# Performance work log

Measured on AMD Instinct MI355X. Metric: run time of the kernel, lower is better.

Reference implementation:

```python
import jax, jax.numpy as jnp
import numpy as np

EMBED_DIM = 1024
NUM_HEADS = 16
HEAD_DIM = EMBED_DIM // NUM_HEADS


def setup_inputs() -> dict:
    key = jax.random.key(0)
    ks = jax.random.split(key, 9)
    B, S, E = 2, 2048, EMBED_DIM
    scale = 1.0 / np.sqrt(E)
    return {
        "query": jax.random.normal(ks[0], (B, S, E), jnp.float32),
        "key": jax.random.normal(ks[1], (B, S, E), jnp.float32),
        "value": jax.random.normal(ks[2], (B, S, E), jnp.float32),
        "wq": jax.random.normal(ks[3], (E, E), jnp.float32) * scale,
        "bq": jnp.zeros((E,), jnp.float32),
        "wk": jax.random.normal(ks[4], (E, E), jnp.float32) * scale,
        "bk": jnp.zeros((E,), jnp.float32),
        "wv": jax.random.normal(ks[5], (E, E), jnp.float32) * scale,
        "bv": jnp.zeros((E,), jnp.float32),
    }


def _split_heads(x):
    B, S, _ = x.shape
    return x.reshape(B, S, NUM_HEADS, HEAD_DIM).transpose(0, 2, 1, 3)  # [B,H,S,Dh]


def reference(query, key, value, wq, bq, wk, bk, wv, bv):
    q = _split_heads(query @ wq + bq)   # [B,H,S,Dh]
    k = _split_heads(key @ wk + bk)
    v = _split_heads(value @ wv + bv)
    logits = jnp.einsum("bhqd,bhkd->bhqk", q, k) / jnp.sqrt(
        jnp.asarray(HEAD_DIM, q.dtype)
    )
    attn = jax.nn.softmax(logits, axis=-1)          # [B,H,S,S]
    out = jnp.einsum("bhqk,bhkd->bhqd", attn, v)    # [B,H,S,Dh]
    B, H, S, Dh = out.shape
    out = out.transpose(0, 2, 1, 3).reshape(B, S, H * Dh)  # [B,S,E]
    return out, attn
```

## Files before the change

kernel.cpp:

```cpp
#include <hip/hip_runtime.h>

typedef float  f32x4  __attribute__((ext_vector_type(4)));
typedef int    i32x4  __attribute__((ext_vector_type(4)));
typedef short  bf16x8 __attribute__((ext_vector_type(8)));
typedef short  s16x4  __attribute__((ext_vector_type(4)));

#define NB   2
#define SEQ  2048
#define EMB  1024
#define NH   16
#define DH   64
#define MATN (NB * SEQ * EMB)

__device__ inline short f2bf(float f) {
    unsigned u = __float_as_uint(f);
    u += 0x7fffu + ((u >> 16) & 1u);
    return (short)(u >> 16);
}

__device__ inline unsigned cvtpk(float lo, float hi) {
    unsigned r;
    asm("v_cvt_pk_bf16_f32 %0, %1, %2" : "=v"(r) : "v"(lo), "v"(hi));
    return r;
}

__device__ inline float fexp2(float x) {
#if __has_builtin(__builtin_amdgcn_exp2f)
    return __builtin_amdgcn_exp2f(x);
#else
    return exp2f(x);
#endif
}

__device__ inline f32x4 mfma16(bf16x8 a, bf16x8 b, f32x4 c) {
    return __builtin_amdgcn_mfma_f32_16x16x32_bf16(a, b, c, 0, 0, 0);
}

__global__ __launch_bounds__(256) void prep_kernel(const float* __restrict__ q,
                                                   const float* __restrict__ k,
                                                   const float* __restrict__ v,
                                                   const float* __restrict__ w0,
                                                   const float* __restrict__ w1,
                                                   const float* __restrict__ w2,
                                                   short* __restrict__ wt,
                                                   short* __restrict__ abf) {
    int blk = blockIdx.x;
    int t = threadIdx.x;
    if (blk < 3072) {
        __shared__ float tile[32][33];
        int mat = blk >> 10;
        int rem = blk & 1023;
        int kt = rem >> 5, nt = rem & 31;
        const float* W = (mat == 0) ? w0 : ((mat == 1) ? w1 : w2);
        int row = t >> 3, c4 = (t & 7) << 2;

        f32x4 val = *(const f32x4*)(W + (kt * 32 + row) * EMB + nt * 32 + c4);
        tile[row][c4 + 0] = val[0];
        tile[row][c4 + 1] = val[1];
        tile[row][c4 + 2] = val[2];
        tile[row][c4 + 3] = val[3];
        __syncthreads();

        int n = nt * 32 + row;
        s16x4 o;
        o[0] = f2bf(tile[c4 + 0][row]);
        o[1] = f2bf(tile[c4 + 1][row]);
        o[2] = f2bf(tile[c4 + 2][row]);
        o[3] = f2bf(tile[c4 + 3][row]);
        *(s16x4*)(wt + mat * (EMB * EMB) + n * EMB + kt * 32 + c4) = o;
    } else {
        long long i = (long long)(blk - 3072) * 2048 + t * 8;
        int mat = (int)(i >> 22);
        int off = (int)(i & (MATN - 1));
        const float* A = (mat == 0) ? q : ((mat == 1) ? k : v);
        f32x4 x = *(const f32x4*)(A + off);
        f32x4 y = *(const f32x4*)(A + off + 4);
        bf16x8 pk;
        pk[0] = f2bf(x[0]); pk[1] = f2bf(x[1]); pk[2] = f2bf(x[2]); pk[3] = f2bf(x[3]);
        pk[4] = f2bf(y[0]); pk[5] = f2bf(y[1]); pk[6] = f2bf(y[2]); pk[7] = f2bf(y[3]);
        *(bf16x8*)(abf + i) = pk;
    }
}

template <bool BF16A>
__global__ __launch_bounds__(256) void proj_kernel(const short* __restrict__ abf,
                                                   const float* __restrict__ a0,
                                                   const float* __restrict__ a1,
                                                   const float* __restrict__ a2,
                                                   const float* __restrict__ b0,
                                                   const float* __restrict__ b1,
                                                   const float* __restrict__ b2,
                                                   const short* __restrict__ wt,
                                                   short* __restrict__ qkv) {
    __shared__ __align__(16) short smem[2][128][72];
    short (*abuf)[72] = smem[0];
    short (*wbuf)[72] = smem[1];

    int orig = blockIdx.x;
    int blk = (orig & 7) * 96 + (orig >> 3);
    int mat = blk >> 8;
    int rem = blk & 255;
    int mt = rem >> 3, nt = rem & 7;

    const float* bias = (mat == 0) ? b0 : ((mat == 1) ? b1 : b2);
    const float* Af = (mat == 0) ? a0 : ((mat == 1) ? a1 : a2);
    const short* Ab = abf + mat * MATN;
    const short* WT = wt + mat * (EMB * EMB);
    short* O = qkv + mat * MATN;
    float scale = (mat == 0) ? 0.125f * 1.44269504f : 1.0f;

    int t = threadIdx.x;
    int lane = t & 63, w = t >> 6;
    int wr = w >> 1, wc = w & 1;
    int lg = lane >> 4, lm = lane & 15;

    int m0 = mt * 128, n0 = nt * 128;
    int srow = t >> 1, koff = (t & 1) * 32;

    f32x4 acc[4][4] = {};

    for (int k0 = 0; k0 < EMB; k0 += 64) {
        if constexpr (BF16A) {
            const short* ap = Ab + (m0 + srow) * EMB + k0 + koff;
#pragma unroll
            for (int i = 0; i < 4; i++)
                *(i32x4*)&abuf[srow][koff + i * 8] = *(const i32x4*)(ap + i * 8);
        } else {
            const float* ap = Af + (m0 + srow) * EMB + k0 + koff;
#pragma unroll
            for (int i = 0; i < 4; i++) {
                f32x4 x = *(const f32x4*)(ap + i * 8);
                f32x4 y = *(const f32x4*)(ap + i * 8 + 4);
                bf16x8 pk;
                pk[0] = f2bf(x[0]); pk[1] = f2bf(x[1]); pk[2] = f2bf(x[2]); pk[3] = f2bf(x[3]);
                pk[4] = f2bf(y[0]); pk[5] = f2bf(y[1]); pk[6] = f2bf(y[2]); pk[7] = f2bf(y[3]);
                *(bf16x8*)&abuf[srow][koff + i * 8] = pk;
            }
        }
        const short* wp = WT + (n0 + srow) * EMB + k0 + koff;
#pragma unroll
        for (int i = 0; i < 4; i++)
            *(i32x4*)&wbuf[srow][koff + i * 8] = *(const i32x4*)(wp + i * 8);
        __syncthreads();
#pragma unroll
        for (int ks = 0; ks < 2; ks++) {
            bf16x8 af[4], bfr[4];
#pragma unroll
            for (int mi = 0; mi < 4; mi++)
                af[mi] = *(const bf16x8*)&abuf[wr * 64 + mi * 16 + lm][ks * 32 + lg * 8];
#pragma unroll
            for (int ni = 0; ni < 4; ni++)
                bfr[ni] = *(const bf16x8*)&wbuf[wc * 64 + ni * 16 + lm][ks * 32 + lg * 8];
#pragma unroll
            for (int mi = 0; mi < 4; mi++)
#pragma unroll
                for (int ni = 0; ni < 4; ni++)
                    acc[mi][ni] = mfma16(af[mi], bfr[ni], acc[mi][ni]);
        }
        __syncthreads();
    }

    int bidx = m0 >> 11;
    if (mat == 2) {
#pragma unroll
        for (int ni = 0; ni < 4; ni++) {
            int e = n0 + wc * 64 + ni * 16 + lm;
            float bv = bias[e];
            int h = e >> 6, d = e & 63;
#pragma unroll
            for (int mi = 0; mi < 4; mi++) {
                int s = (m0 + wr * 64 + mi * 16 + lg * 4) & (SEQ - 1);
                s16x4 o;
#pragma unroll
                for (int r = 0; r < 4; r++) o[r] = f2bf(acc[mi][ni][r] + bv);
                *(s16x4*)(O + (((bidx * NH + h) * DH + d) * SEQ) + s) = o;
            }
        }
    } else {
        short* flat = &smem[0][0][0];
#pragma unroll
        for (int ni = 0; ni < 4; ni++) {
            int e = n0 + wc * 64 + ni * 16 + lm;
            float bv = bias[e];
#pragma unroll
            for (int mi = 0; mi < 4; mi++) {
                int rr = wr * 64 + mi * 16 + lg * 4;
#pragma unroll
                for (int r = 0; r < 4; r++)
                    flat[(rr + r) * 136 + wc * 64 + ni * 16 + lm] =
                        f2bf((acc[mi][ni][r] + bv) * scale);
            }
        }
        __syncthreads();
        int r = t >> 1, half = t & 1;
        int h = (n0 + half * 64) >> 6;
        int s = (m0 + r) & (SEQ - 1);
        short* dst = O + (((long long)bidx * NH + h) * SEQ + s) * DH;
        const short* srcp = flat + r * 136 + half * 64;
#pragma unroll
        for (int j = 0; j < 8; j++)
            *(i32x4*)(dst + j * 8) = *(const i32x4*)(srcp + j * 8);
    }
}

__global__ __launch_bounds__(256) void attn_kernel(const short* __restrict__ qkv,
                                                   float* __restrict__ out,
                                                   float* __restrict__ attn) {
    const short* Qb = qkv;
    const short* Kb = qkv + MATN;
    const short* Vt = qkv + 2 * MATN;

    __shared__ __align__(16) short kbuf[2][64][72];
    __shared__ __align__(16) short vbuf[2][4096];

    int orig = blockIdx.x;
    int wg = (orig & 7) * 128 + (orig >> 3);
    int bh = wg >> 5;
    int q0 = (wg & 31) * 64;
    int b = bh >> 4, hq = bh & 15;

    int t = threadIdx.x, lane = t & 63, w = t >> 6;
    int lg = lane >> 4, lm = lane & 15;
    int srow = t >> 2, sch = t & 3;

    {
        const short* qp = Qb + (bh * SEQ + q0 + srow) * DH + sch * 16;
        *(i32x4*)&kbuf[0][srow][sch * 16]     = *(const i32x4*)(qp);
        *(i32x4*)&kbuf[0][srow][sch * 16 + 8] = *(const i32x4*)(qp + 8);
    }
    __syncthreads();
    bf16x8 qf[2];
    {
        int myq = w * 16 + lm;
        qf[0] = *(const bf16x8*)&kbuf[0][myq][lg * 8];
        qf[1] = *(const bf16x8*)&kbuf[0][myq][32 + lg * 8];
    }
    __syncthreads();

    const short* kbase = Kb + (long long)bh * SEQ * DH;
    const short* vbase = Vt + (long long)bh * DH * SEQ;

    i32x4 kr0, kr1;
    {
        const short* kp = kbase + srow * DH + sch * 16;
        kr0 = *(const i32x4*)(kp); kr1 = *(const i32x4*)(kp + 8);
    }
    float rsum = 0.0f;
    for (int kt = 0; kt < 32; kt++) {
        *(i32x4*)&kbuf[kt & 1][srow][sch * 16]     = kr0;
        *(i32x4*)&kbuf[kt & 1][srow][sch * 16 + 8] = kr1;
        __syncthreads();
        if (kt < 31) {
            const short* kp = kbase + ((kt + 1) * 64 + srow) * DH + sch * 16;
            kr0 = *(const i32x4*)(kp); kr1 = *(const i32x4*)(kp + 8);
        }
#pragma unroll
        for (int ki = 0; ki < 4; ki++) {
            f32x4 s = {};
            bf16x8 kf0 = *(const bf16x8*)&kbuf[kt & 1][ki * 16 + lm][lg * 8];
            bf16x8 kf1 = *(const bf16x8*)&kbuf[kt & 1][ki * 16 + lm][32 + lg * 8];
            s = mfma16(kf0, qf[0], s);
            s = mfma16(kf1, qf[1], s);
            rsum += fexp2(s[0]) + fexp2(s[1]) + fexp2(s[2]) + fexp2(s[3]);
        }
    }
    rsum += __shfl_xor(rsum, 16);
    rsum += __shfl_xor(rsum, 32);
    float inv = 1.0f / rsum;

    f32x4 oacc[4] = {};
    float* arow = attn + ((long long)bh * SEQ + q0 + w * 16 + lm) * SEQ;

    int vA0 = (srow >> 4) * 1024 + (sch >> 1) * 512 + (srow & 15) * 8 + (sch & 1) * 4;

    i32x4 vr0, vr1;
    {
        const short* kp = kbase + srow * DH + sch * 16;
        kr0 = *(const i32x4*)(kp); kr1 = *(const i32x4*)(kp + 8);
        const short* vp = vbase + srow * SEQ + sch * 16;
        vr0 = *(const i32x4*)(vp); vr1 = *(const i32x4*)(vp + 8);
    }

    for (int kt = 0; kt < 32; kt++) {
        *(i32x4*)&kbuf[kt & 1][srow][sch * 16]     = kr0;
        *(i32x4*)&kbuf[kt & 1][srow][sch * 16 + 8] = kr1;
        union { i32x4 v; s16x4 h[2]; } u0, u1;
        u0.v = vr0; u1.v = vr1;
        *(s16x4*)&vbuf[kt & 1][vA0]       = u0.h[0];
        *(s16x4*)&vbuf[kt & 1][vA0 + 128] = u0.h[1];
        *(s16x4*)&vbuf[kt & 1][vA0 + 256] = u1.h[0];
        *(s16x4*)&vbuf[kt & 1][vA0 + 384] = u1.h[1];
        __syncthreads();
        if (kt < 31) {
            const short* kp = kbase + ((kt + 1) * 64 + srow) * DH + sch * 16;
            kr0 = *(const i32x4*)(kp); kr1 = *(const i32x4*)(kp + 8);
            const short* vp = vbase + srow * SEQ + (kt + 1) * 64 + sch * 16;
            vr0 = *(const i32x4*)(vp); vr1 = *(const i32x4*)(vp + 8);
        }

        float p[4][4];
#pragma unroll
        for (int ki = 0; ki < 4; ki++) {
            f32x4 s = {};
            bf16x8 kf0 = *(const bf16x8*)&kbuf[kt & 1][ki * 16 + lm][lg * 8];
            bf16x8 kf1 = *(const bf16x8*)&kbuf[kt & 1][ki * 16 + lm][32 + lg * 8];
            s = mfma16(kf0, qf[0], s);
            s = mfma16(kf1, qf[1], s);
#pragma unroll
            for (int r = 0; r < 4; r++) p[ki][r] = fexp2(s[r]) * inv;
            f32x4 st = {p[ki][0], p[ki][1], p[ki][2], p[ki][3]};
            __builtin_nontemporal_store(st, (f32x4*)(arow + kt * 64 + ki * 16 + lg * 4));
        }

        bf16x8 pb[2];
#pragma unroll
        for (int ks = 0; ks < 2; ks++) {
            union { unsigned d[4]; bf16x8 v; } u;
            u.d[0] = cvtpk(p[2 * ks + 0][0], p[2 * ks + 0][1]);
            u.d[1] = cvtpk(p[2 * ks + 0][2], p[2 * ks + 0][3]);
            u.d[2] = cvtpk(p[2 * ks + 1][0], p[2 * ks + 1][1]);
            u.d[3] = cvtpk(p[2 * ks + 1][2], p[2 * ks + 1][3]);
            pb[ks] = u.v;
        }

#pragma unroll
        for (int di = 0; di < 4; di++) {
#pragma unroll
            for (int ks = 0; ks < 2; ks++) {
                bf16x8 vf = *(const bf16x8*)&vbuf[kt & 1][(di * 2 + ks) * 512 + (lg * 16 + lm) * 8];
                oacc[di] = mfma16(vf, pb[ks], oacc[di]);
            }
        }
    }

    float* op = out + ((long long)b * SEQ + q0 + w * 16 + lm) * EMB + hq * DH;
#pragma unroll
    for (int di = 0; di < 4; di++) {
        __builtin_nontemporal_store(oacc[di], (f32x4*)(op + di * 16 + lg * 4));
    }
}

extern "C" void kernel_launch(void* const* d_in, const int* in_sizes, int n_in,
                              void* d_out, int out_size, void* d_ws, size_t ws_size,
                              hipStream_t stream) {
    const float* query = (const float*)d_in[0];
    const float* key   = (const float*)d_in[1];
    const float* value = (const float*)d_in[2];
    const float* wq    = (const float*)d_in[3];
    const float* bq    = (const float*)d_in[4];
    const float* wk    = (const float*)d_in[5];
    const float* bk    = (const float*)d_in[6];
    const float* wv    = (const float*)d_in[7];
    const float* bv    = (const float*)d_in[8];

    float* out  = (float*)d_out;
    float* attn = out + (long long)NB * SEQ * EMB;

    size_t need_full = ((size_t)3 * EMB * EMB + 6ull * MATN) * sizeof(short);
    bool bf16a = ws_size >= need_full;

    short* wt  = (short*)d_ws;
    short* abf = wt + 3 * (EMB * EMB);
    short* qkv = bf16a ? (abf + 3 * MATN) : abf;

    hipLaunchKernelGGL(prep_kernel, dim3(bf16a ? 9216 : 3072), dim3(256), 0, stream,
                       query, key, value, wq, wk, wv, wt, abf);
    if (bf16a) {
        hipLaunchKernelGGL((proj_kernel<true>), dim3(768), dim3(256), 0, stream,
                           abf, query, key, value, bq, bk, bv, wt, qkv);
    } else {
        hipLaunchKernelGGL((proj_kernel<false>), dim3(768), dim3(256), 0, stream,
                           abf, query, key, value, bq, bk, bv, wt, qkv);
    }
    hipLaunchKernelGGL(attn_kernel, dim3(1024), dim3(256), 0, stream,
                       qkv, out, attn);
}
```

Baseline: 268.8 us.

## Load MFMA operands directly from global memory, dropping LDS staging for projection and K

The projection GEMM no longer stages A and W tiles through shared memory. Each wave now loads its own MFMA fragments straight from global memory, which removes the per-k-step barriers. In the attention kernel, Q and K fragments are likewise read directly from global memory instead of through a double-buffered kbuf, and only V stays staged in LDS. This trades LDS traffic and synchronisation for redundant global/L2 reads, since each wave fetches operands that were previously shared across waves, and it loses the coalesced, software-prefetched loads.

```diff
diff --git a/kernel.cpp b/kernel.cpp
--- a/kernel.cpp
+++ b/kernel.cpp
@@ -92,9 +92,7 @@
                                                    const float* __restrict__ b2,
                                                    const short* __restrict__ wt,
                                                    short* __restrict__ qkv) {
-    __shared__ __align__(16) short smem[2][128][72];
-    short (*abuf)[72] = smem[0];
-    short (*wbuf)[72] = smem[1];
+    __shared__ __align__(16) short flat[128 * 136];
 
     int orig = blockIdx.x;
     int blk = (orig & 7) * 96 + (orig >> 3);
@@ -115,49 +113,60 @@
     int lg = lane >> 4, lm = lane & 15;
 
     int m0 = mt * 128, n0 = nt * 128;
-    int srow = t >> 1, koff = (t & 1) * 32;
+
+    const short* wp[4];
+#pragma unroll
+    for (int ni = 0; ni < 4; ni++)
+        wp[ni] = WT + (n0 + wc * 64 + ni * 16 + lm) * EMB + lg * 8;
 
     f32x4 acc[4][4] = {};
 
-    for (int k0 = 0; k0 < EMB; k0 += 64) {
-        if constexpr (BF16A) {
-            const short* ap = Ab + (m0 + srow) * EMB + k0 + koff;
-#pragma unroll
-            for (int i = 0; i < 4; i++)
-                *(i32x4*)&abuf[srow][koff + i * 8] = *(const i32x4*)(ap + i * 8);
-        } else {
-            const float* ap = Af + (m0 + srow) * EMB + k0 + koff;
-#pragma unroll
-            for (int i = 0; i < 4; i++) {
-                f32x4 x = *(const f32x4*)(ap + i * 8);
-                f32x4 y = *(const f32x4*)(ap + i * 8 + 4);
+    if constexpr (BF16A) {
+        const short* ap[4];
+#pragma unroll
+        for (int mi = 0; mi < 4; mi++)
+            ap[mi] = Ab + (m0 + wr * 64 + mi * 16 + lm) * EMB + lg * 8;
+#pragma unroll 2
+        for (int k0 = 0; k0 < EMB; k0 += 32) {
+            bf16x8 af[4], bfr[4];
+#pragma unroll
+            for (int mi = 0; mi < 4; mi++)
+                af[mi] = *(const bf16x8*)(ap[mi] + k0);
+#pragma unroll
+            for (int ni = 0; ni < 4; ni++)
+                bfr[ni] = *(const bf16x8*)(wp[ni] + k0);
+#pragma unroll
+            for (int mi = 0; mi < 4; mi++)
+#pragma unroll
+                for (int ni = 0; ni < 4; ni++)
+                    acc[mi][ni] = mfma16(af[mi], bfr[ni], acc[mi][ni]);
+        }
+    } else {
+        const float* apf[4];
+#pragma unroll
+        for (int mi = 0; mi < 4; mi++)
+            apf[mi] = Af + (m0 + wr * 64 + mi * 16 + lm) * EMB + lg * 8;
+#pragma unroll 2
+        for (int k0 = 0; k0 < EMB; k0 += 32) {
+            bf16x8 af[4], bfr[4];
+#pragma unroll
+            for (int mi = 0; mi < 4; mi++) {
+                f32x4 x = *(const f32x4*)(apf[mi] + k0);
+                f32x4 y = *(const f32x4*)(apf[mi] + k0 + 4);
                 bf16x8 pk;
                 pk[0] = f2bf(x[0]); pk[1] = f2bf(x[1]); pk[2] = f2bf(x[2]); pk[3] = f2bf(x[3]);
                 pk[4] = f2bf(y[0]); pk[5] = f2bf(y[1]); pk[6] = f2bf(y[2]); pk[7] = f2bf(y[3]);
-                *(bf16x8*)&abuf[srow][koff + i * 8] = pk;
+                af[mi] = pk;
             }
-        }
-        const short* wp = WT + (n0 + srow) * EMB + k0 + koff;
-#pragma unroll
-        for (int i = 0; i < 4; i++)
-            *(i32x4*)&wbuf[srow][koff + i * 8] = *(const i32x4*)(wp + i * 8);
-        __syncthreads();
-#pragma unroll
-        for (int ks = 0; ks < 2; ks++) {
-            bf16x8 af[4], bfr[4];
-#pragma unroll
-            for (int mi = 0; mi < 4; mi++)
-                af[mi] = *(const bf16x8*)&abuf[wr * 64 + mi * 16 + lm][ks * 32 + lg * 8];
 #pragma unroll
             for (int ni = 0; ni < 4; ni++)
-                bfr[ni] = *(const bf16x8*)&wbuf[wc * 64 + ni * 16 + lm][ks * 32 + lg * 8];
+                bfr[ni] = *(const bf16x8*)(wp[ni] + k0);
 #pragma unroll
             for (int mi = 0; mi < 4; mi++)
 #pragma unroll
                 for (int ni = 0; ni < 4; ni++)
                     acc[mi][ni] = mfma16(af[mi], bfr[ni], acc[mi][ni]);
         }
-        __syncthreads();
     }
 
     int bidx = m0 >> 11;
@@ -177,7 +186,6 @@
             }
         }
     } else {
-        short* flat = &smem[0][0][0];
 #pragma unroll
         for (int ni = 0; ni < 4; ni++) {
             int e = n0 + wc * 64 + ni * 16 + lm;
@@ -210,7 +218,6 @@
     const short* Kb = qkv + MATN;
     const short* Vt = qkv + 2 * MATN;
 
-    __shared__ __align__(16) short kbuf[2][64][72];
     __shared__ __align__(16) short vbuf[2][4096];
 
     int orig = blockIdx.x;
@@ -223,44 +230,27 @@
     int lg = lane >> 4, lm = lane & 15;
     int srow = t >> 2, sch = t & 3;
 
-    {
-        const short* qp = Qb + (bh * SEQ + q0 + srow) * DH + sch * 16;
-        *(i32x4*)&kbuf[0][srow][sch * 16]     = *(const i32x4*)(qp);
-        *(i32x4*)&kbuf[0][srow][sch * 16 + 8] = *(const i32x4*)(qp + 8);
-    }
-    __syncthreads();
-    bf16x8 qf[2];
-    {
-        int myq = w * 16 + lm;
-        qf[0] = *(const bf16x8*)&kbuf[0][myq][lg * 8];
-        qf[1] = *(const bf16x8*)&kbuf[0][myq][32 + lg * 8];
-    }
-    __syncthreads();
-
     const short* kbase = Kb + (long long)bh * SEQ * DH;
     const short* vbase = Vt + (long long)bh * DH * SEQ;
 
-    i32x4 kr0, kr1;
+    bf16x8 qf0, qf1;
     {
-        const short* kp = kbase + srow * DH + sch * 16;
-        kr0 = *(const i32x4*)(kp); kr1 = *(const i32x4*)(kp + 8);
-    }
+        const short* qrow = Qb + ((long long)bh * SEQ + q0 + w * 16 + lm) * DH + lg * 8;
+        qf0 = *(const bf16x8*)(qrow);
+        qf1 = *(const bf16x8*)(qrow + 32);
+    }
+
     float rsum = 0.0f;
+#pragma unroll 2
     for (int kt = 0; kt < 32; kt++) {
-        *(i32x4*)&kbuf[kt & 1][srow][sch * 16]     = kr0;
-        *(i32x4*)&kbuf[kt & 1][srow][sch * 16 + 8] = kr1;
-        __syncthreads();
-        if (kt < 31) {
-            const short* kp = kbase + ((kt + 1) * 64 + srow) * DH + sch * 16;
-            kr0 = *(const i32x4*)(kp); kr1 = *(const i32x4*)(kp + 8);
-        }
+        const short* kp = kbase + (kt * 64 + lm) * DH + lg * 8;
 #pragma unroll
         for (int ki = 0; ki < 4; ki++) {
             f32x4 s = {};
-            bf16x8 kf0 = *(const bf16x8*)&kbuf[kt & 1][ki * 16 + lm][lg * 8];
-            bf16x8 kf1 = *(const bf16x8*)&kbuf[kt & 1][ki * 16 + lm][32 + lg * 8];
-            s = mfma16(kf0, qf[0], s);
-            s = mfma16(kf1, qf[1], s);
+            bf16x8 kf0 = *(const bf16x8*)(kp + ki * 16 * DH);
+            bf16x8 kf1 = *(const bf16x8*)(kp + ki * 16 * DH + 32);
+            s = mfma16(kf0, qf0, s);
+            s = mfma16(kf1, qf1, s);
             rsum += fexp2(s[0]) + fexp2(s[1]) + fexp2(s[2]) + fexp2(s[3]);
         }
     }
@@ -275,15 +265,11 @@
 
     i32x4 vr0, vr1;
     {
-        const short* kp = kbase + srow * DH + sch * 16;
-        kr0 = *(const i32x4*)(kp); kr1 = *(const i32x4*)(kp + 8);
         const short* vp = vbase + srow * SEQ + sch * 16;
         vr0 = *(const i32x4*)(vp); vr1 = *(const i32x4*)(vp + 8);
     }
 
     for (int kt = 0; kt < 32; kt++) {
-        *(i32x4*)&kbuf[kt & 1][srow][sch * 16]     = kr0;
-        *(i32x4*)&kbuf[kt & 1][srow][sch * 16 + 8] = kr1;
         union { i32x4 v; s16x4 h[2]; } u0, u1;
         u0.v = vr0; u1.v = vr1;
         *(s16x4*)&vbuf[kt & 1][vA0]       = u0.h[0];
@@ -292,20 +278,19 @@
         *(s16x4*)&vbuf[kt & 1][vA0 + 384] = u1.h[1];
         __syncthreads();
         if (kt < 31) {
-            const short* kp = kbase + ((kt + 1) * 64 + srow) * DH + sch * 16;
-            kr0 = *(const i32x4*)(kp); kr1 = *(const i32x4*)(kp + 8);
             const short* vp = vbase + srow * SEQ + (kt + 1) * 64 + sch * 16;
             vr0 = *(const i32x4*)(vp); vr1 = *(const i32x4*)(vp + 8);
         }
 
+        const short* kp = kbase + (kt * 64 + lm) * DH + lg * 8;
         float p[4][4];
 #pragma unroll
         for (int ki = 0; ki < 4; ki++) {
             f32x4 s = {};
-            bf16x8 kf0 = *(const bf16x8*)&kbuf[kt & 1][ki * 16 + lm][lg * 8];
-            bf16x8 kf1 = *(const bf16x8*)&kbuf[kt & 1][ki * 16 + lm][32 + lg * 8];
-            s = mfma16(kf0, qf[0], s);
-            s = mfma16(kf1, qf[1], s);
+            bf16x8 kf0 = *(const bf16x8*)(kp + ki * 16 * DH);
+            bf16x8 kf1 = *(const bf16x8*)(kp + ki * 16 * DH + 32);
+            s = mfma16(kf0, qf0, s);
+            s = mfma16(kf1, qf1, s);
 #pragma unroll
             for (int r = 0; r < 4; r++) p[ki][r] = fexp2(s[r]) * inv;
             f32x4 st = {p[ki][0], p[ki][1], p[ki][2], p[ki][3]};
```

After: 468.0 us. 74.1% more time.

## Enlarge attention workgroups to 128 queries with 512 threads sharing K/V tiles

Applied to the files above, without the earlier changes.

The attention kernel now runs 512 workgroups of 512 threads, each covering 128 query rows instead of 64. Each K/V tile staged in shared memory therefore serves eight waves, halving global K/V traffic per query. Each thread loads one 16-byte chunk per tile instead of two, and Q fragments are read straight from global memory instead of through LDS. The trade-off is fewer workgroups, which risks lower occupancy and worse load balance, plus barriers spanning more waves.

```diff
diff --git a/kernel.cpp b/kernel.cpp
--- a/kernel.cpp
+++ b/kernel.cpp
@@ -203,7 +203,7 @@
     }
 }
 
-__global__ __launch_bounds__(256) void attn_kernel(const short* __restrict__ qkv,
+__global__ __launch_bounds__(512) void attn_kernel(const short* __restrict__ qkv,
                                                    float* __restrict__ out,
                                                    float* __restrict__ attn) {
     const short* Qb = qkv;
@@ -214,53 +214,40 @@
     __shared__ __align__(16) short vbuf[2][4096];
 
     int orig = blockIdx.x;
-    int wg = (orig & 7) * 128 + (orig >> 3);
-    int bh = wg >> 5;
-    int q0 = (wg & 31) * 64;
+    int wg = (orig & 7) * 64 + (orig >> 3);
+    int bh = wg >> 4;
+    int q0 = (wg & 15) * 128;
     int b = bh >> 4, hq = bh & 15;
 
     int t = threadIdx.x, lane = t & 63, w = t >> 6;
     int lg = lane >> 4, lm = lane & 15;
-    int srow = t >> 2, sch = t & 3;
-
-    {
-        const short* qp = Qb + (bh * SEQ + q0 + srow) * DH + sch * 16;
-        *(i32x4*)&kbuf[0][srow][sch * 16]     = *(const i32x4*)(qp);
-        *(i32x4*)&kbuf[0][srow][sch * 16 + 8] = *(const i32x4*)(qp + 8);
-    }
-    __syncthreads();
-    bf16x8 qf[2];
-    {
-        int myq = w * 16 + lm;
-        qf[0] = *(const bf16x8*)&kbuf[0][myq][lg * 8];
-        qf[1] = *(const bf16x8*)&kbuf[0][myq][32 + lg * 8];
-    }
-    __syncthreads();
+    int srow = t >> 3, sc = t & 7;
 
     const short* kbase = Kb + (long long)bh * SEQ * DH;
     const short* vbase = Vt + (long long)bh * DH * SEQ;
 
-    i32x4 kr0, kr1;
+    bf16x8 qf0, qf1;
     {
-        const short* kp = kbase + srow * DH + sch * 16;
-        kr0 = *(const i32x4*)(kp); kr1 = *(const i32x4*)(kp + 8);
-    }
+        const short* qrow = Qb + ((long long)bh * SEQ + q0 + w * 16 + lm) * DH + lg * 8;
+        qf0 = *(const bf16x8*)(qrow);
+        qf1 = *(const bf16x8*)(qrow + 32);
+    }
+
+    i32x4 kr;
+    kr = *(const i32x4*)(kbase + srow * DH + sc * 8);
     float rsum = 0.0f;
     for (int kt = 0; kt < 32; kt++) {
-        *(i32x4*)&kbuf[kt & 1][srow][sch * 16]     = kr0;
-        *(i32x4*)&kbuf[kt & 1][srow][sch * 16 + 8] = kr1;
-        __syncthreads();
-        if (kt < 31) {
-            const short* kp = kbase + ((kt + 1) * 64 + srow) * DH + sch * 16;
-            kr0 = *(const i32x4*)(kp); kr1 = *(const i32x4*)(kp + 8);
-        }
+        *(i32x4*)&kbuf[kt & 1][srow][sc * 8] = kr;
+        __syncthreads();
+        if (kt < 31)
+            kr = *(const i32x4*)(kbase + ((kt + 1) * 64 + srow) * DH + sc * 8);
 #pragma unroll
         for (int ki = 0; ki < 4; ki++) {
             f32x4 s = {};
             bf16x8 kf0 = *(const bf16x8*)&kbuf[kt & 1][ki * 16 + lm][lg * 8];
             bf16x8 kf1 = *(const bf16x8*)&kbuf[kt & 1][ki * 16 + lm][32 + lg * 8];
-            s = mfma16(kf0, qf[0], s);
-            s = mfma16(kf1, qf[1], s);
+            s = mfma16(kf0, qf0, s);
+            s = mfma16(kf1, qf1, s);
             rsum += fexp2(s[0]) + fexp2(s[1]) + fexp2(s[2]) + fexp2(s[3]);
         }
     }
@@ -271,31 +258,25 @@
     f32x4 oacc[4] = {};
     float* arow = attn + ((long long)bh * SEQ + q0 + w * 16 + lm) * SEQ;
 
-    int vA0 = (srow >> 4) * 1024 + (sch >> 1) * 512 + (srow & 15) * 8 + (sch & 1) * 4;
-
-    i32x4 vr0, vr1;
+    int vA0 = (srow >> 4) * 1024 + (sc >> 2) * 512 + (sc & 1) * 256
+            + (srow & 15) * 8 + ((sc >> 1) & 1) * 4;
+
+    i32x4 vr;
     {
-        const short* kp = kbase + srow * DH + sch * 16;
-        kr0 = *(const i32x4*)(kp); kr1 = *(const i32x4*)(kp + 8);
-        const short* vp = vbase + srow * SEQ + sch * 16;
-        vr0 = *(const i32x4*)(vp); vr1 = *(const i32x4*)(vp + 8);
+        kr = *(const i32x4*)(kbase + srow * DH + sc * 8);
+        vr = *(const i32x4*)(vbase + srow * SEQ + sc * 8);
     }
 
     for (int kt = 0; kt < 32; kt++) {
-        *(i32x4*)&kbuf[kt & 1][srow][sch * 16]     = kr0;
-        *(i32x4*)&kbuf[kt & 1][srow][sch * 16 + 8] = kr1;
-        union { i32x4 v; s16x4 h[2]; } u0, u1;
-        u0.v = vr0; u1.v = vr1;
-        *(s16x4*)&vbuf[kt & 1][vA0]       = u0.h[0];
-        *(s16x4*)&vbuf[kt & 1][vA0 + 128] = u0.h[1];
-        *(s16x4*)&vbuf[kt & 1][vA0 + 256] = u1.h[0];
-        *(s16x4*)&vbuf[kt & 1][vA0 + 384] = u1.h[1];
+        *(i32x4*)&kbuf[kt & 1][srow][sc * 8] = kr;
+        union { i32x4 v; s16x4 h[2]; } u;
+        u.v = vr;
+        *(s16x4*)&vbuf[kt & 1][vA0]       = u.h[0];
+        *(s16x4*)&vbuf[kt & 1][vA0 + 128] = u.h[1];
         __syncthreads();
         if (kt < 31) {
-            const short* kp = kbase + ((kt + 1) * 64 + srow) * DH + sch * 16;
-            kr0 = *(const i32x4*)(kp); kr1 = *(const i32x4*)(kp + 8);
-            const short* vp = vbase + srow * SEQ + (kt + 1) * 64 + sch * 16;
-            vr0 = *(const i32x4*)(vp); vr1 = *(const i32x4*)(vp + 8);
+            kr = *(const i32x4*)(kbase + ((kt + 1) * 64 + srow) * DH + sc * 8);
+            vr = *(const i32x4*)(vbase + srow * SEQ + (kt + 1) * 64 + sc * 8);
         }
 
         float p[4][4];
@@ -304,8 +285,8 @@
             f32x4 s = {};
             bf16x8 kf0 = *(const bf16x8*)&kbuf[kt & 1][ki * 16 + lm][lg * 8];
             bf16x8 kf1 = *(const bf16x8*)&kbuf[kt & 1][ki * 16 + lm][32 + lg * 8];
-            s = mfma16(kf0, qf[0], s);
-            s = mfma16(kf1, qf[1], s);
+            s = mfma16(kf0, qf0, s);
+            s = mfma16(kf1, qf1, s);
 #pragma unroll
             for (int r = 0; r < 4; r++) p[ki][r] = fexp2(s[r]) * inv;
             f32x4 st = {p[ki][0], p[ki][1], p[ki][2], p[ki][3]};
@@ -315,12 +296,12 @@
         bf16x8 pb[2];
 #pragma unroll
         for (int ks = 0; ks < 2; ks++) {
-            union { unsigned d[4]; bf16x8 v; } u;
-            u.d[0] = cvtpk(p[2 * ks + 0][0], p[2 * ks + 0][1]);
-            u.d[1] = cvtpk(p[2 * ks + 0][2], p[2 * ks + 0][3]);
-            u.d[2] = cvtpk(p[2 * ks + 1][0], p[2 * ks + 1][1]);
-            u.d[3] = cvtpk(p[2 * ks + 1][2], p[2 * ks + 1][3]);
-            pb[ks] = u.v;
+            union { unsigned d[4]; bf16x8 v; } up;
+            up.d[0] = cvtpk(p[2 * ks + 0][0], p[2 * ks + 0][1]);
+            up.d[1] = cvtpk(p[2 * ks + 0][2], p[2 * ks + 0][3]);
+            up.d[2] = cvtpk(p[2 * ks + 1][0], p[2 * ks + 1][1]);
+            up.d[3] = cvtpk(p[2 * ks + 1][2], p[2 * ks + 1][3]);
+            pb[ks] = up.v;
         }
 
 #pragma unroll
@@ -372,6 +353,6 @@
         hipLaunchKernelGGL((proj_kernel<false>), dim3(768), dim3(256), 0, stream,
                            abf, query, key, value, bq, bk, bv, wt, qkv);
     }
-    hipLaunchKernelGGL(attn_kernel, dim3(1024), dim3(256), 0, stream,
+    hipLaunchKernelGGL(attn_kernel, dim3(512), dim3(512), 0, stream,
                        qkv, out, attn);
 }
```

Result: slower. 276.4 us (+2.8%).

## Use direct global-to-LDS loads with XOR swizzle in projection, load Q directly, set MFMA priority

Applied to the files above, without the earlier changes.

The bf16 projection path now stages A and W tiles with global_load_lds straight into LDS, using an unpadded layout with an XOR swizzle on 16-byte chunks to avoid bank conflicts. This removes the VGPR round trip and the padding. The attention kernel now loads Q fragments directly from global memory instead of staging them through LDS with two barriers. It also wraps the MFMA sequences in s_setprio to favour matrix issue across waves. The projection still uses single buffering, so load latency stays exposed, and the priority hints may or may not help scheduling.

```diff
diff --git a/kernel.cpp b/kernel.cpp
--- a/kernel.cpp
+++ b/kernel.cpp
@@ -34,6 +34,12 @@
 
 __device__ inline f32x4 mfma16(bf16x8 a, bf16x8 b, f32x4 c) {
     return __builtin_amdgcn_mfma_f32_16x16x32_bf16(a, b, c, 0, 0, 0);
+}
+
+__device__ inline void gload_lds16(const short* g, short* l) {
+    __builtin_amdgcn_global_load_lds(
+        (const __attribute__((address_space(1))) void*)g,
+        (__attribute__((address_space(3))) void*)l, 16, 0, 0);
 }
 
 __global__ __launch_bounds__(256) void prep_kernel(const float* __restrict__ q,
@@ -92,9 +98,7 @@
                                                    const float* __restrict__ b2,
                                                    const short* __restrict__ wt,
                                                    short* __restrict__ qkv) {
-    __shared__ __align__(16) short smem[2][128][72];
-    short (*abuf)[72] = smem[0];
-    short (*wbuf)[72] = smem[1];
+    __shared__ __align__(16) short smem[18432];
 
     int orig = blockIdx.x;
     int blk = (orig & 7) * 96 + (orig >> 3);
@@ -115,17 +119,51 @@
     int lg = lane >> 4, lm = lane & 15;
 
     int m0 = mt * 128, n0 = nt * 128;
-    int srow = t >> 1, koff = (t & 1) * 32;
 
     f32x4 acc[4][4] = {};
 
-    for (int k0 = 0; k0 < EMB; k0 += 64) {
-        if constexpr (BF16A) {
-            const short* ap = Ab + (m0 + srow) * EMB + k0 + koff;
-#pragma unroll
-            for (int i = 0; i < 4; i++)
-                *(i32x4*)&abuf[srow][koff + i * 8] = *(const i32x4*)(ap + i * 8);
-        } else {
+    if constexpr (BF16A) {
+        const short* gA[4];
+        const short* gW[4];
+        int ldso[4];
+#pragma unroll
+        for (int i = 0; i < 4; i++) {
+            int u = w * 256 + i * 64 + lane;
+            int row = u >> 3;
+            int c = (u & 7) ^ (row & 7);
+            gA[i] = Ab + (m0 + row) * EMB + c * 8;
+            gW[i] = WT + (n0 + row) * EMB + c * 8;
+            ldso[i] = (w * 256 + i * 64) * 8;
+        }
+        int xr = lm & 7;
+        for (int k0 = 0; k0 < EMB; k0 += 64) {
+#pragma unroll
+            for (int i = 0; i < 4; i++) {
+                gload_lds16(gA[i] + k0, smem + ldso[i]);
+                gload_lds16(gW[i] + k0, smem + 8192 + ldso[i]);
+            }
+            __syncthreads();
+#pragma unroll
+            for (int ks = 0; ks < 2; ks++) {
+                bf16x8 af[4], bfr[4];
+                int cc = (ks * 4 + lg) ^ xr;
+#pragma unroll
+                for (int mi = 0; mi < 4; mi++)
+                    af[mi] = *(const bf16x8*)(smem + (wr * 64 + mi * 16 + lm) * 64 + cc * 8);
+#pragma unroll
+                for (int ni = 0; ni < 4; ni++)
+                    bfr[ni] = *(const bf16x8*)(smem + 8192 + (wc * 64 + ni * 16 + lm) * 64 + cc * 8);
+#pragma unroll
+                for (int mi = 0; mi < 4; mi++)
+#pragma unroll
+                    for (int ni = 0; ni < 4; ni++)
+                        acc[mi][ni] = mfma16(af[mi], bfr[ni], acc[mi][ni]);
+            }
+            __syncthreads();
+        }
+    } else {
+        int srow = t >> 1, koff = (t & 1) * 32;
+        for (int k0 = 0; k0 < EMB; k0 += 64) {
             const float* ap = Af + (m0 + srow) * EMB + k0 + koff;
 #pragma unroll
             for (int i = 0; i < 4; i++) {
@@ -134,30 +172,30 @@
                 bf16x8 pk;
                 pk[0] = f2bf(x[0]); pk[1] = f2bf(x[1]); pk[2] = f2bf(x[2]); pk[3] = f2bf(x[3]);
                 pk[4] = f2bf(y[0]); pk[5] = f2bf(y[1]); pk[6] = f2bf(y[2]); pk[7] = f2bf(y[3]);
-                *(bf16x8*)&abuf[srow][koff + i * 8] = pk;
-            }
-        }
-        const short* wp = WT + (n0 + srow) * EMB + k0 + koff;
-#pragma unroll
-        for (int i = 0; i < 4; i++)
-            *(i32x4*)&wbuf[srow][koff + i * 8] = *(const i32x4*)(wp + i * 8);
-        __syncthreads();
-#pragma unroll
-        for (int ks = 0; ks < 2; ks++) {
-            bf16x8 af[4], bfr[4];
-#pragma unroll
-            for (int mi = 0; mi < 4; mi++)
-                af[mi] = *(const bf16x8*)&abuf[wr * 64 + mi * 16 + lm][ks * 32 + lg * 8];
-#pragma unroll
-            for (int ni = 0; ni < 4; ni++)
-                bfr[ni] = *(const bf16x8*)&wbuf[wc * 64 + ni * 16 + lm][ks * 32 + lg * 8];
-#pragma unroll
-            for (int mi = 0; mi < 4; mi++)
+                *(bf16x8*)&smem[srow * 72 + koff + i * 8] = pk;
+            }
+            const short* wp = WT + (n0 + srow) * EMB + k0 + koff;
+#pragma unroll
+            for (int i = 0; i < 4; i++)
+                *(i32x4*)&smem[9216 + srow * 72 + koff + i * 8] = *(const i32x4*)(wp + i * 8);
+            __syncthreads();
+#pragma unroll
+            for (int ks = 0; ks < 2; ks++) {
+                bf16x8 af[4], bfr[4];
+#pragma unroll
+                for (int mi = 0; mi < 4; mi++)
+                    af[mi] = *(const bf16x8*)&smem[(wr * 64 + mi * 16 + lm) * 72 + ks * 32 + lg * 8];
 #pragma unroll
                 for (int ni = 0; ni < 4; ni++)
-                    acc[mi][ni] = mfma16(af[mi], bfr[ni], acc[mi][ni]);
-        }
-        __syncthreads();
+                    bfr[ni] = *(const bf16x8*)&smem[9216 + (wc * 64 + ni * 16 + lm) * 72 + ks * 32 + lg * 8];
+#pragma unroll
+                for (int mi = 0; mi < 4; mi++)
+#pragma unroll
+                    for (int ni = 0; ni < 4; ni++)
+                        acc[mi][ni] = mfma16(af[mi], bfr[ni], acc[mi][ni]);
+            }
+            __syncthreads();
+        }
     }
 
     int bidx = m0 >> 11;
@@ -177,7 +215,6 @@
             }
         }
     } else {
-        short* flat = &smem[0][0][0];
 #pragma unroll
         for (int ni = 0; ni < 4; ni++) {
             int e = n0 + wc * 64 + ni * 16 + lm;
@@ -187,7 +224,7 @@
                 int rr = wr * 64 + mi * 16 + lg * 4;
 #pragma unroll
                 for (int r = 0; r < 4; r++)
-                    flat[(rr + r) * 136 + wc * 64 + ni * 16 + lm] =
+                    smem[(rr + r) * 136 + wc * 64 + ni * 16 + lm] =
                         f2bf((acc[mi][ni][r] + bv) * scale);
             }
         }
@@ -196,7 +233,7 @@
         int h = (n0 + half * 64) >> 6;
         int s = (m0 + r) & (SEQ - 1);
         short* dst = O + (((long long)bidx * NH + h) * SEQ + s) * DH;
-        const short* srcp = flat + r * 136 + half * 64;
+        const short* srcp = smem + r * 136 + half * 64;
 #pragma unroll
         for (int j = 0; j < 8; j++)
             *(i32x4*)(dst + j * 8) = *(const i32x4*)(srcp + j * 8);
@@ -223,22 +260,15 @@
     int lg = lane >> 4, lm = lane & 15;
     int srow = t >> 2, sch = t & 3;
 
-    {
-        const short* qp = Qb + (bh * SEQ + q0 + srow) * DH + sch * 16;
-        *(i32x4*)&kbuf[0][srow][sch * 16]     = *(const i32x4*)(qp);
-        *(i32x4*)&kbuf[0][srow][sch * 16 + 8] = *(const i32x4*)(qp + 8);
-    }
-    __syncthreads();
-    bf16x8 qf[2];
-    {
-        int myq = w * 16 + lm;
-        qf[0] = *(const bf16x8*)&kbuf[0][myq][lg * 8];
-        qf[1] = *(const bf16x8*)&kbuf[0][myq][32 + lg * 8];
-    }
-    __syncthreads();
-
     const short* kbase = Kb + (long long)bh * SEQ * DH;
     const short* vbase = Vt + (long long)bh * DH * SEQ;
+
+    bf16x8 qf0, qf1;
+    {
+        const short* qrow = Qb + ((long long)bh * SEQ + q0 + w * 16 + lm) * DH + lg * 8;
+        qf0 = *(const bf16x8*)(qrow);
+        qf1 = *(const bf16x8*)(qrow + 32);
+    }
 
     i32x4 kr0, kr1;
     {
@@ -259,8 +289,10 @@
             f32x4 s = {};
             bf16x8 kf0 = *(const bf16x8*)&kbuf[kt & 1][ki * 16 + lm][lg * 8];
             bf16x8 kf1 = *(const bf16x8*)&kbuf[kt & 1][ki * 16 + lm][32 + lg * 8];
-            s = mfma16(kf0, qf[0], s);
-            s = mfma16(kf1, qf[1], s);
+            __builtin_amdgcn_s_setprio(1);
+            s = mfma16(kf0, qf0, s);
+            s = mfma16(kf1, qf1, s);
+            __builtin_amdgcn_s_setprio(0);
             rsum += fexp2(s[0]) + fexp2(s[1]) + fexp2(s[2]) + fexp2(s[3]);
         }
     }
@@ -304,8 +336,10 @@
             f32x4 s = {};
             bf16x8 kf0 = *(const bf16x8*)&kbuf[kt & 1][ki * 16 + lm][lg * 8];
             bf16x8 kf1 = *(const bf16x8*)&kbuf[kt & 1][ki * 16 + lm][32 + lg * 8];
-            s = mfma16(kf0, qf[0], s);
-            s = mfma16(kf1, qf[1], s);
+            __builtin_amdgcn_s_setprio(1);
+            s = mfma16(kf0, qf0, s);
+            s = mfma16(kf1, qf1, s);
+            __builtin_amdgcn_s_setprio(0);
 #pragma unroll
             for (int r = 0; r < 4; r++) p[ki][r] = fexp2(s[r]) * inv;
             f32x4 st = {p[ki][0], p[ki][1], p[ki][2], p[ki][3]};
@@ -315,14 +349,15 @@
         bf16x8 pb[2];
 #pragma unroll
         for (int ks = 0; ks < 2; ks++) {
-            union { unsigned d[4]; bf16x8 v; } u;
-            u.d[0] = cvtpk(p[2 * ks + 0][0], p[2 * ks + 0][1]);
-            u.d[1] = cvtpk(p[2 * ks + 0][2], p[2 * ks + 0][3]);
-            u.d[2] = cvtpk(p[2 * ks + 1][0], p[2 * ks + 1][1]);
-            u.d[3] = cvtpk(p[2 * ks + 1][2], p[2 * ks + 1][3]);
-            pb[ks] = u.v;
-        }
-
+            union { unsigned d[4]; bf16x8 v; } up;
+            up.d[0] = cvtpk(p[2 * ks + 0][0], p[2 * ks + 0][1]);
+            up.d[1] = cvtpk(p[2 * ks + 0][2], p[2 * ks + 0][3]);
+            up.d[2] = cvtpk(p[2 * ks + 1][0], p[2 * ks + 1][1]);
+            up.d[3] = cvtpk(p[2 * ks + 1][2], p[2 * ks + 1][3]);
+            pb[ks] = up.v;
+        }
+
+        __builtin_amdgcn_s_setprio(1);
 #pragma unroll
         for (int di = 0; di < 4; di++) {
 #pragma unroll
@@ -331,6 +366,7 @@
                 oacc[di] = mfma16(vf, pb[ks], oacc[di]);
             }
         }
+        __builtin_amdgcn_s_setprio(0);
     }
 
     float* op = out + ((long long)b * SEQ + q0 + w * 16 + lm) * EMB + hq * DH;
```

After: 260.6 us. 1.03x faster.
